# Kernel tuning notes

Measured on AMD Instinct MI355X. Metric: run time of the kernel, lower is better.

Reference implementation:

```python
import jax, jax.numpy as jnp
import numpy as np

N_NODES = 50000
N_EDGES = 500000
D = 128
R = 8
L = 2
BN_EPS = 1e-5


def setup_inputs() -> dict:
    key = jax.random.key(0)
    ks = jax.random.split(key, 8)
    x = jax.random.normal(ks[0], (N_NODES, D), dtype=jnp.float32)
    xe = jax.random.normal(ks[1], (N_EDGES, D), dtype=jnp.float32)
    edge_index = jax.random.randint(ks[2], (2, N_EDGES), 0, N_NODES, dtype=jnp.int64)
    edge_type = jax.random.randint(ks[3], (N_EDGES,), 0, R, dtype=jnp.int64)
    # glorot init for weight/root, zeros bias; BN affine params
    w_scale = jnp.sqrt(6.0 / (D + D))
    weight = jax.random.uniform(ks[4], (L, R, D, D), jnp.float32, -w_scale, w_scale)
    root = jax.random.uniform(ks[5], (L, D, D), jnp.float32, -w_scale, w_scale)
    bias = jnp.zeros((L, D), jnp.float32)
    bn_gamma = jnp.ones((L, D), jnp.float32)
    bn_beta = jnp.zeros((L, D), jnp.float32)
    return {"x": x, "xe": xe, "edge_index": edge_index, "edge_type": edge_type,
            "weight": weight, "root": root, "bias": bias,
            "bn_gamma": bn_gamma, "bn_beta": bn_beta}


def _rgcn_edge_conv(h, xe, src, dst, etype, w, rt, b):
    # message: relu(x_j + xe) per edge (independent of relation mask)
    m = jax.nn.relu(h[src] + xe)                         # [E, D]
    # mean-aggregate per (relation, dst) via a combined segment id
    n = h.shape[0]
    seg = etype * n + dst                                # [E]
    sums = jax.ops.segment_sum(m, seg, num_segments=R * n)            # [R*N, D]
    cnt = jax.ops.segment_sum(jnp.ones((m.shape[0],), m.dtype), seg,
                              num_segments=R * n)                     # [R*N]
    mean = sums / jnp.maximum(cnt, 1.0)[:, None]
    hr = mean.reshape(R, n, -1)                          # [R, N, D]
    out = jnp.einsum('rnd,rdo->no', hr, w)               # sum_i H_i @ W_i
    out = out + h @ rt + b
    return out


def _batch_norm(h, gamma, beta):
    mu = h.mean(axis=0)
    var = jnp.mean((h - mu) ** 2, axis=0)  # biased, as torch BN (training)
    return (h - mu) * jax.lax.rsqrt(var + BN_EPS) * gamma + beta


def reference(x, xe, edge_index, edge_type, weight, root, bias, bn_gamma, bn_beta):
    src, dst = edge_index[0], edge_index[1]
    h = x
    for l in range(L):
        h = _rgcn_edge_conv(h, xe, src, dst, edge_type, weight[l], root[l], bias[l])
        h = _batch_norm(h, bn_gamma[l], bn_beta[l])
        if l != L - 1:
            h = jax.nn.relu(h)
        # drop_ratio=0 -> dropout is identity
    return h  # JK='last'
```

## Files before the change

kernel.cpp:

```cpp
#include <hip/hip_runtime.h>
#include <hip/hip_bf16.h>

typedef __attribute__((ext_vector_type(8))) short bf16x8;
typedef __attribute__((ext_vector_type(4))) float f32x4;

constexpr int D = 128;
constexpr int R = 8;
constexpr float BN_EPS = 1e-5f;

__device__ __forceinline__ unsigned short f2bf(float x) {
  __hip_bfloat16 b = __float2bfloat16(x);
  union { __hip_bfloat16 b; unsigned short u; } c; c.b = b; return c.u;
}
__device__ __forceinline__ float bf2f(unsigned short u) {
  union { float f; unsigned int i; } c; c.i = ((unsigned int)u) << 16; return c.f;
}

__global__ __launch_bounds__(256) void hist_k(const int* __restrict__ ei,
                                              const int* __restrict__ et,
                                              int* __restrict__ cnt, int E) {
  int e = blockIdx.x * 256 + threadIdx.x;
  if (e >= E) return;
  atomicAdd(&cnt[ei[E + e] * 8 + et[e]], 1);
}

__global__ __launch_bounds__(256) void scan_partial_k(const int* __restrict__ cnt,
                                                      int* __restrict__ offs,
                                                      int* __restrict__ bsum, int NK) {
  __shared__ int s[256];
  int tid = threadIdx.x;
  int base = blockIdx.x * 4096 + tid * 16;
  int loc[16];
  int sum = 0;
  #pragma unroll
  for (int i = 0; i < 16; ++i) {
    int idx = base + i;
    int v = (idx < NK) ? cnt[idx] : 0;
    loc[i] = sum; sum += v;
  }
  s[tid] = sum;
  __syncthreads();
  if (tid == 0) {
    int run = 0;
    for (int i = 0; i < 256; ++i) { int t = s[i]; s[i] = run; run += t; }
    bsum[blockIdx.x] = run;
  }
  __syncthreads();
  int off = s[tid];
  #pragma unroll
  for (int i = 0; i < 16; ++i) {
    int idx = base + i;
    if (idx < NK) offs[idx] = off + loc[i];
  }
}

__global__ void scan_bsums_k(int* __restrict__ bsum, int nb) {
  if (threadIdx.x == 0 && blockIdx.x == 0) {
    int run = 0;
    for (int b = 0; b < nb; ++b) { int t = bsum[b]; bsum[b] = run; run += t; }
  }
}

__global__ __launch_bounds__(256) void scan_addback_k(int* __restrict__ offs,
                                                      const int* __restrict__ bsum,
                                                      int NK, int E) {
  int idx = blockIdx.x * 256 + threadIdx.x;
  if (idx < NK) offs[idx] += bsum[idx >> 12];
  if (idx == 0) offs[NK] = E;
}

__global__ __launch_bounds__(256) void place_k(const int* __restrict__ ei,
                                               const int* __restrict__ et,
                                               const int* __restrict__ offs,
                                               int* __restrict__ cnt,
                                               int2* __restrict__ pairs, int E) {
  int e = blockIdx.x * 256 + threadIdx.x;
  if (e >= E) return;
  int key = ei[E + e] * 8 + et[e];
  int pos = offs[key] + atomicAdd(&cnt[key], 1);
  pairs[pos] = make_int2(e, ei[e]);
}

__global__ void bnprep_k(const float* __restrict__ colstats,
                         const float* __restrict__ gamma,
                         const float* __restrict__ beta,
                         float* __restrict__ sc, float* __restrict__ sh, int N) {
  int c = threadIdx.x;
  float invN = 1.0f / (float)N;
  float mu = colstats[c] * invN;
  float var = colstats[128 + c] * invN - mu * mu;
  float scale = rsqrtf(var + BN_EPS) * gamma[c];
  sc[c] = scale;
  sh[c] = beta[c] - mu * scale;
}

__device__ __forceinline__ void edge_acc(float4& acc, int e, int s, int c, int pos,
                                         const unsigned short* __restrict__ hb,
                                         const float* __restrict__ xe) {
  float4 xv = ((const float4*)xe)[(size_t)e * 32 + c];
  ushort4 hu = *(const ushort4*)(hb + (size_t)s * 128 + pos);
  acc.x += fmaxf(xv.x + bf2f(hu.x), 0.f);
  acc.y += fmaxf(xv.y + bf2f(hu.y), 0.f);
  acc.z += fmaxf(xv.z + bf2f(hu.z), 0.f);
  acc.w += fmaxf(xv.w + bf2f(hu.w), 0.f);
}

__global__ __launch_bounds__(256) void agg_k(const unsigned short* __restrict__ hb,
                                             const float* __restrict__ xe,
                                             const int2* __restrict__ pairs,
                                             const int* __restrict__ offs,
                                             unsigned short* __restrict__ Mb,
                                             int NK, int rev) {
  int grp = threadIdx.x >> 5;
  int idx = blockIdx.x * 8 + grp;
  int nIdx = NK >> 3;
  if (idx >= nIdx) return;
  if (rev) idx = nIdx - 1 - idx;
  int s0 = idx * 8;
  int c = threadIdx.x & 31;
  int pos = (c >> 3) * 32 + (c & 3) * 8 + ((c >> 2) & 1) * 4;

  int4 ov0 = *(const int4*)(offs + s0);
  int4 ov1 = *(const int4*)(offs + s0 + 4);
  int o8 = offs[s0 + 8];
  int st[8] = {ov0.x, ov0.y, ov0.z, ov0.w, ov1.x, ov1.y, ov1.z, ov1.w};
  int en[8] = {ov0.y, ov0.z, ov0.w, ov1.x, ov1.y, ov1.z, ov1.w, o8};

  int2 pr[8];
  #pragma unroll
  for (int j = 0; j < 8; ++j) {
    int m = en[j] - st[j];
    if (m > 0) pr[j] = pairs[st[j] + min(c, min(m, 32) - 1)];
  }

  float4 acc[8];
  #pragma unroll
  for (int j = 0; j < 8; ++j) acc[j] = make_float4(0.f, 0.f, 0.f, 0.f);

#define EP(j, i) edge_acc(acc[j], __shfl(pr[j].x, (i), 32), \
                          __shfl(pr[j].y, (i), 32), c, pos, hb, xe)

  #pragma unroll
  for (int j = 0; j < 8; ++j) {
    int m = en[j] - st[j];
    if (m > 0) {
      int mm = min(m, 32);
      EP(j, 0);
      if (mm >= 2) EP(j, 1);
      if (mm >= 3) EP(j, 2);
      if (mm >= 4) EP(j, 3);
      for (int i = 4; i < mm; ++i) EP(j, i);
      for (int base = st[j] + 32; base < en[j]; base += 32) {
        int mm2 = min(32, en[j] - base);
        int2 pr2 = pairs[base + min(c, mm2 - 1)];
        for (int i = 0; i < mm2; ++i)
          edge_acc(acc[j], __shfl(pr2.x, i, 32), __shfl(pr2.y, i, 32),
                   c, pos, hb, xe);
      }
    }
  }
#undef EP

  #pragma unroll
  for (int j = 0; j < 8; ++j) {
    int len = en[j] - st[j];
    float inv = (len > 0) ? 1.0f / (float)len : 0.f;
    ushort4 u;
    u.x = f2bf(acc[j].x * inv); u.y = f2bf(acc[j].y * inv);
    u.z = f2bf(acc[j].z * inv); u.w = f2bf(acc[j].w * inv);
    *(ushort4*)(Mb + (size_t)(s0 + j) * 128 + pos) = u;
  }
}

template <int AFF>
__global__ __launch_bounds__(256) void cast_swz_k(const float* __restrict__ in,
                                                  unsigned short* __restrict__ outb,
                                                  const float* __restrict__ sc,
                                                  const float* __restrict__ sh,
                                                  int n4) {
  int gi = blockIdx.x * 256 + threadIdx.x;
  if (gi >= n4) return;
  int n = gi >> 5, c = gi & 31;
  float4 v = ((const float4*)in)[gi];
  if (AFF) {
    float4 scv = *(const float4*)(sc + c * 4);
    float4 shv = *(const float4*)(sh + c * 4);
    v.x = fmaxf(fmaf(v.x, scv.x, shv.x), 0.f);
    v.y = fmaxf(fmaf(v.y, scv.y, shv.y), 0.f);
    v.z = fmaxf(fmaf(v.z, scv.z, shv.z), 0.f);
    v.w = fmaxf(fmaf(v.w, scv.w, shv.w), 0.f);
  }
  int pos = (c >> 3) * 32 + (c & 3) * 8 + ((c >> 2) & 1) * 4;
  ushort4 u;
  u.x = f2bf(v.x); u.y = f2bf(v.y); u.z = f2bf(v.z); u.w = f2bf(v.w);
  *(ushort4*)(outb + (size_t)n * 128 + pos) = u;
}

__global__ __launch_bounds__(256) void wcast_k(const float* __restrict__ W,
                                               const float* __restrict__ root,
                                               unsigned short* __restrict__ Whi) {
  int idx = blockIdx.x * 256 + threadIdx.x;
  if (idx >= 1152 * 128) return;
  int k = idx >> 7, col = idx & 127;
  float w = (k < 1024) ? W[idx] : root[idx - 1024 * 128];
  int kk = k & 31;
  int pos = (k & ~31) + ((kk & 15) >> 2) * 8 + (kk >> 4) * 4 + (kk & 3);
  Whi[col * 1152 + pos] = f2bf(w);
}

__global__ __launch_bounds__(256) void gemm_k(
    const unsigned short* __restrict__ Mb,
    const unsigned short* __restrict__ hb,
    const unsigned short* __restrict__ Whi,
    const float* __restrict__ bias,
    float* __restrict__ out,
    float* __restrict__ colstats, int N) {
  __shared__ float ldsS[128], ldsQ[128];
  const int tid = threadIdx.x;
  const int wv = tid >> 6, lane = tid & 63;
  const int lr = lane & 15, g = lane >> 4;
  const int r0 = blockIdx.x * 128;
  const int cf0 = wv * 2;

  int row[8];
  #pragma unroll
  for (int rf = 0; rf < 8; ++rf) row[rf] = min(r0 + rf * 16 + lr, N - 1);

  const unsigned short* pb0 = Whi + (size_t)(cf0 * 16 + lr) * 1152 + g * 8;
  const unsigned short* pb1 = pb0 + 16 * 1152;

  f32x4 acc[8][2];
  #pragma unroll
  for (int a = 0; a < 8; ++a)
    #pragma unroll
    for (int b = 0; b < 2; ++b) acc[a][b] = (f32x4){0.f, 0.f, 0.f, 0.f};

  #pragma unroll 2
  for (int t = 0; t < 32; ++t) {
    bf16x8 b0 = *(const bf16x8*)(pb0 + t * 32);
    bf16x8 b1 = *(const bf16x8*)(pb1 + t * 32);
    #pragma unroll
    for (int rf = 0; rf < 8; ++rf) {
      bf16x8 a = *(const bf16x8*)(Mb + (size_t)row[rf] * 1024 + t * 32 + g * 8);
      acc[rf][0] = __builtin_amdgcn_mfma_f32_16x16x32_bf16(a, b0, acc[rf][0], 0, 0, 0);
      acc[rf][1] = __builtin_amdgcn_mfma_f32_16x16x32_bf16(a, b1, acc[rf][1], 0, 0, 0);
    }
  }
  #pragma unroll
  for (int tt = 0; tt < 4; ++tt) {
    bf16x8 b0 = *(const bf16x8*)(pb0 + 1024 + tt * 32);
    bf16x8 b1 = *(const bf16x8*)(pb1 + 1024 + tt * 32);
    #pragma unroll
    for (int rf = 0; rf < 8; ++rf) {
      bf16x8 a = *(const bf16x8*)(hb + (size_t)row[rf] * 128 + tt * 32 + g * 8);
      acc[rf][0] = __builtin_amdgcn_mfma_f32_16x16x32_bf16(a, b0, acc[rf][0], 0, 0, 0);
      acc[rf][1] = __builtin_amdgcn_mfma_f32_16x16x32_bf16(a, b1, acc[rf][1], 0, 0, 0);
    }
  }

  #pragma unroll
  for (int c = 0; c < 2; ++c) {
    int col = (cf0 + c) * 16 + lr;
    float bs = bias[col];
    float s = 0.f, q = 0.f;
    #pragma unroll
    for (int rf = 0; rf < 8; ++rf) {
      #pragma unroll
      for (int j = 0; j < 4; ++j) {
        int r = r0 + rf * 16 + g * 4 + j;
        if (r < N) {
          float v = acc[rf][c][j] + bs;
          out[(size_t)r * 128 + col] = v;
          s += v; q += v * v;
        }
      }
    }
    s += __shfl_xor(s, 16); s += __shfl_xor(s, 32);
    q += __shfl_xor(q, 16); q += __shfl_xor(q, 32);
    if (g == 0) { ldsS[col] = s; ldsQ[col] = q; }
  }
  __syncthreads();
  if (tid < 128) {
    atomicAdd(&colstats[tid], ldsS[tid]);
    atomicAdd(&colstats[128 + tid], ldsQ[tid]);
  }
}

__global__ __launch_bounds__(256) void bn_apply_k(
    const float* __restrict__ in, float* __restrict__ out,
    const float* __restrict__ colstats,
    const float* __restrict__ gamma, const float* __restrict__ beta, int N) {
  int gi = blockIdx.x * 256 + threadIdx.x;
  if (gi >= N * 32) return;
  int c0 = (gi & 31) * 4;
  float invN = 1.0f / (float)N;
  float4 v = ((const float4*)in)[gi];
  float4 o;
  #pragma unroll
  for (int j = 0; j < 4; ++j) {
    int cc = c0 + j;
    float mu = colstats[cc] * invN;
    float var = colstats[128 + cc] * invN - mu * mu;
    float scale = rsqrtf(var + BN_EPS) * gamma[cc];
    float shift = beta[cc] - mu * scale;
    float x = (j == 0) ? v.x : (j == 1) ? v.y : (j == 2) ? v.z : v.w;
    float y = x * scale + shift;
    if (j == 0) o.x = y; else if (j == 1) o.y = y; else if (j == 2) o.z = y; else o.w = y;
  }
  ((float4*)out)[gi] = o;
}

extern "C" void kernel_launch(void* const* d_in, const int* in_sizes, int n_in,
                              void* d_out, int out_size, void* d_ws, size_t ws_size,
                              hipStream_t stream) {
  const float* x      = (const float*)d_in[0];
  const float* xe     = (const float*)d_in[1];
  const int*   ei     = (const int*)d_in[2];
  const int*   et     = (const int*)d_in[3];
  const float* weight = (const float*)d_in[4];
  const float* root   = (const float*)d_in[5];
  const float* bias   = (const float*)d_in[6];
  const float* gamma  = (const float*)d_in[7];
  const float* beta   = (const float*)d_in[8];
  float* out = (float*)d_out;

  const int N = in_sizes[0] / D;
  const int E = in_sizes[3];
  const int NK = N * R;

  char* w = (char*)d_ws;
  size_t off = 0;
  auto alloc = [&](size_t bytes) { char* p = w + off; off = (off + bytes + 255) & ~(size_t)255; return p; };
  unsigned short* Mb   = (unsigned short*)alloc((size_t)NK * 128 * 2);
  unsigned short* hb   = (unsigned short*)alloc((size_t)N * 128 * 2);
  float*          h1   = (float*)alloc((size_t)N * 128 * 4);
  unsigned short* Whi  = (unsigned short*)alloc(1152 * 128 * 2);
  int*            offs = (int*)alloc((size_t)(NK + 8) * 4);
  int*            cnt  = (int*)alloc((size_t)NK * 4);
  int2*           pairs= (int2*)alloc((size_t)E * 8);
  int*            bsum = (int*)alloc(512 * 4);
  float*          cst0 = (float*)alloc(256 * 4);
  float*          cst1 = (float*)alloc(256 * 4);
  float*          sc   = (float*)alloc(128 * 4);
  float*          sh   = (float*)alloc(128 * 4);

  const int NB = (NK + 4095) / 4096;

  hipMemsetAsync(cnt, 0, (size_t)NK * 4, stream);
  hist_k<<<(E + 255) / 256, 256, 0, stream>>>(ei, et, cnt, E);
  scan_partial_k<<<NB, 256, 0, stream>>>(cnt, offs, bsum, NK);
  scan_bsums_k<<<1, 64, 0, stream>>>(bsum, NB);
  scan_addback_k<<<(NK + 255) / 256, 256, 0, stream>>>(offs, bsum, NK, E);
  hipMemsetAsync(cnt, 0, (size_t)NK * 4, stream);
  place_k<<<(E + 255) / 256, 256, 0, stream>>>(ei, et, offs, cnt, pairs, E);

  const int aggBlocks  = ((NK >> 3) + 7) / 8;
  const int gemmBlocks = (N + 127) / 128;
  const int castBlocks = (N * 32 + 255) / 256;

  wcast_k<<<576, 256, 0, stream>>>(weight, root, Whi);
  cast_swz_k<0><<<castBlocks, 256, 0, stream>>>(x, hb, nullptr, nullptr, N * 32);
  agg_k<<<aggBlocks, 256, 0, stream>>>(hb, xe, pairs, offs, Mb, NK, 0);
  hipMemsetAsync(cst0, 0, 256 * 4, stream);
  gemm_k<<<gemmBlocks, 256, 0, stream>>>(Mb, hb, Whi, bias, h1, cst0, N);
  bnprep_k<<<1, 128, 0, stream>>>(cst0, gamma, beta, sc, sh, N);

  wcast_k<<<576, 256, 0, stream>>>(weight + (size_t)1024 * 128,
                                   root + (size_t)128 * 128, Whi);
  cast_swz_k<1><<<castBlocks, 256, 0, stream>>>(h1, hb, sc, sh, N * 32);
  agg_k<<<aggBlocks, 256, 0, stream>>>(hb, xe, pairs, offs, Mb, NK, 1);
  hipMemsetAsync(cst1, 0, 256 * 4, stream);
  gemm_k<<<gemmBlocks, 256, 0, stream>>>(Mb, hb, Whi, bias + D, out, cst1, N);
  bn_apply_k<<<castBlocks, 256, 0, stream>>>(out, out, cst1, gamma + D, beta + D, N);
}
```

Baseline: 471.0 us.

## Split edge aggregation into coalesced message pass and segment reduce, gather in GEMM

Reorders segment keys to relation-major, replaces the per-segment gather kernel with a per-edge message kernel that reads xe sequentially and scatters bf16 messages into sorted slots, then a reduce kernel that only averages segments with two or more edges. The GEMM reads each relation's A rows indirectly from a zero row, the single message, or the reduced mean, avoiding writes for empty and singleton segments. This trades random xe reads for an extra bf16 message buffer write and read and indirect A loads in the GEMM.

```diff
diff --git a/kernel.cpp b/kernel.cpp
--- a/kernel.cpp
+++ b/kernel.cpp
@@ -15,13 +15,16 @@
 __device__ __forceinline__ float bf2f(unsigned short u) {
   union { float f; unsigned int i; } c; c.i = ((unsigned int)u) << 16; return c.f;
 }
+__device__ __forceinline__ int swz(int c) {
+  return (c >> 3) * 32 + (c & 3) * 8 + ((c >> 2) & 1) * 4;
+}
 
 __global__ __launch_bounds__(256) void hist_k(const int* __restrict__ ei,
                                               const int* __restrict__ et,
-                                              int* __restrict__ cnt, int E) {
+                                              int* __restrict__ cnt, int E, int N) {
   int e = blockIdx.x * 256 + threadIdx.x;
   if (e >= E) return;
-  atomicAdd(&cnt[ei[E + e] * 8 + et[e]], 1);
+  atomicAdd(&cnt[et[e] * N + ei[E + e]], 1);
 }
 
 __global__ __launch_bounds__(256) void scan_partial_k(const int* __restrict__ cnt,
@@ -73,12 +76,11 @@
                                                const int* __restrict__ et,
                                                const int* __restrict__ offs,
                                                int* __restrict__ cnt,
-                                               int2* __restrict__ pairs, int E) {
+                                               int* __restrict__ epos, int E, int N) {
   int e = blockIdx.x * 256 + threadIdx.x;
   if (e >= E) return;
-  int key = ei[E + e] * 8 + et[e];
-  int pos = offs[key] + atomicAdd(&cnt[key], 1);
-  pairs[pos] = make_int2(e, ei[e]);
+  int key = et[e] * N + ei[E + e];
+  epos[e] = offs[key] + atomicAdd(&cnt[key], 1);
 }
 
 __global__ void bnprep_k(const float* __restrict__ colstats,
@@ -94,31 +96,37 @@
   sh[c] = beta[c] - mu * scale;
 }
 
-__device__ __forceinline__ void edge_acc(float4& acc, int e, int s, int c, int pos,
-                                         const unsigned short* __restrict__ hb,
-                                         const float* __restrict__ xe) {
+__global__ __launch_bounds__(256) void msg_k(const unsigned short* __restrict__ hb,
+                                             const float* __restrict__ xe,
+                                             const int* __restrict__ ei,
+                                             const int* __restrict__ epos,
+                                             unsigned short* __restrict__ msgs, int E) {
+  int g = blockIdx.x * 256 + threadIdx.x;
+  int e = g >> 5, c = g & 31;
+  if (e >= E) return;
+  int src = ei[e];
+  int p = epos[e];
+  int pos = swz(c);
   float4 xv = ((const float4*)xe)[(size_t)e * 32 + c];
-  ushort4 hu = *(const ushort4*)(hb + (size_t)s * 128 + pos);
-  acc.x += fmaxf(xv.x + bf2f(hu.x), 0.f);
-  acc.y += fmaxf(xv.y + bf2f(hu.y), 0.f);
-  acc.z += fmaxf(xv.z + bf2f(hu.z), 0.f);
-  acc.w += fmaxf(xv.w + bf2f(hu.w), 0.f);
-}
-
-__global__ __launch_bounds__(256) void agg_k(const unsigned short* __restrict__ hb,
-                                             const float* __restrict__ xe,
-                                             const int2* __restrict__ pairs,
-                                             const int* __restrict__ offs,
-                                             unsigned short* __restrict__ Mb,
-                                             int NK, int rev) {
+  ushort4 hu = *(const ushort4*)(hb + (size_t)src * 128 + pos);
+  ushort4 u;
+  u.x = f2bf(fmaxf(xv.x + bf2f(hu.x), 0.f));
+  u.y = f2bf(fmaxf(xv.y + bf2f(hu.y), 0.f));
+  u.z = f2bf(fmaxf(xv.z + bf2f(hu.z), 0.f));
+  u.w = f2bf(fmaxf(xv.w + bf2f(hu.w), 0.f));
+  *(ushort4*)(msgs + (size_t)p * 128 + pos) = u;
+}
+
+__global__ __launch_bounds__(256) void reduce_k(const unsigned short* __restrict__ msgs,
+                                                const int* __restrict__ offs,
+                                                unsigned short* __restrict__ Mb, int NK) {
   int grp = threadIdx.x >> 5;
   int idx = blockIdx.x * 8 + grp;
   int nIdx = NK >> 3;
   if (idx >= nIdx) return;
-  if (rev) idx = nIdx - 1 - idx;
   int s0 = idx * 8;
   int c = threadIdx.x & 31;
-  int pos = (c >> 3) * 32 + (c & 3) * 8 + ((c >> 2) & 1) * 4;
+  int pos = swz(c);
 
   int4 ov0 = *(const int4*)(offs + s0);
   int4 ov1 = *(const int4*)(offs + s0 + 4);
@@ -126,49 +134,22 @@
   int st[8] = {ov0.x, ov0.y, ov0.z, ov0.w, ov1.x, ov1.y, ov1.z, ov1.w};
   int en[8] = {ov0.y, ov0.z, ov0.w, ov1.x, ov1.y, ov1.z, ov1.w, o8};
 
-  int2 pr[8];
-  #pragma unroll
-  for (int j = 0; j < 8; ++j) {
-    int m = en[j] - st[j];
-    if (m > 0) pr[j] = pairs[st[j] + min(c, min(m, 32) - 1)];
-  }
-
-  float4 acc[8];
-  #pragma unroll
-  for (int j = 0; j < 8; ++j) acc[j] = make_float4(0.f, 0.f, 0.f, 0.f);
-
-#define EP(j, i) edge_acc(acc[j], __shfl(pr[j].x, (i), 32), \
-                          __shfl(pr[j].y, (i), 32), c, pos, hb, xe)
-
-  #pragma unroll
-  for (int j = 0; j < 8; ++j) {
-    int m = en[j] - st[j];
-    if (m > 0) {
-      int mm = min(m, 32);
-      EP(j, 0);
-      if (mm >= 2) EP(j, 1);
-      if (mm >= 3) EP(j, 2);
-      if (mm >= 4) EP(j, 3);
-      for (int i = 4; i < mm; ++i) EP(j, i);
-      for (int base = st[j] + 32; base < en[j]; base += 32) {
-        int mm2 = min(32, en[j] - base);
-        int2 pr2 = pairs[base + min(c, mm2 - 1)];
-        for (int i = 0; i < mm2; ++i)
-          edge_acc(acc[j], __shfl(pr2.x, i, 32), __shfl(pr2.y, i, 32),
-                   c, pos, hb, xe);
-      }
-    }
-  }
-#undef EP
-
   #pragma unroll
   for (int j = 0; j < 8; ++j) {
     int len = en[j] - st[j];
-    float inv = (len > 0) ? 1.0f / (float)len : 0.f;
-    ushort4 u;
-    u.x = f2bf(acc[j].x * inv); u.y = f2bf(acc[j].y * inv);
-    u.z = f2bf(acc[j].z * inv); u.w = f2bf(acc[j].w * inv);
-    *(ushort4*)(Mb + (size_t)(s0 + j) * 128 + pos) = u;
+    if (len >= 2) {
+      float4 acc = make_float4(0.f, 0.f, 0.f, 0.f);
+      for (int i = st[j]; i < en[j]; ++i) {
+        ushort4 u = *(const ushort4*)(msgs + (size_t)i * 128 + pos);
+        acc.x += bf2f(u.x); acc.y += bf2f(u.y);
+        acc.z += bf2f(u.z); acc.w += bf2f(u.w);
+      }
+      float inv = 1.0f / (float)len;
+      ushort4 o;
+      o.x = f2bf(acc.x * inv); o.y = f2bf(acc.y * inv);
+      o.z = f2bf(acc.z * inv); o.w = f2bf(acc.w * inv);
+      *(ushort4*)(Mb + (size_t)(s0 + j) * 128 + pos) = o;
+    }
   }
 }
 
@@ -190,7 +171,7 @@
     v.z = fmaxf(fmaf(v.z, scv.z, shv.z), 0.f);
     v.w = fmaxf(fmaf(v.w, scv.w, shv.w), 0.f);
   }
-  int pos = (c >> 3) * 32 + (c & 3) * 8 + ((c >> 2) & 1) * 4;
+  int pos = swz(c);
   ushort4 u;
   u.x = f2bf(v.x); u.y = f2bf(v.y); u.z = f2bf(v.z); u.w = f2bf(v.w);
   *(ushort4*)(outb + (size_t)n * 128 + pos) = u;
@@ -209,7 +190,10 @@
 }
 
 __global__ __launch_bounds__(256) void gemm_k(
+    const unsigned short* __restrict__ msgs,
     const unsigned short* __restrict__ Mb,
+    const int* __restrict__ offs,
+    const unsigned short* __restrict__ zrow,
     const unsigned short* __restrict__ hb,
     const unsigned short* __restrict__ Whi,
     const float* __restrict__ bias,
@@ -235,15 +219,28 @@
     #pragma unroll
     for (int b = 0; b < 2; ++b) acc[a][b] = (f32x4){0.f, 0.f, 0.f, 0.f};
 
-  #pragma unroll 2
-  for (int t = 0; t < 32; ++t) {
-    bf16x8 b0 = *(const bf16x8*)(pb0 + t * 32);
-    bf16x8 b1 = *(const bf16x8*)(pb1 + t * 32);
+  for (int rel = 0; rel < 8; ++rel) {
+    const unsigned short* base[8];
     #pragma unroll
     for (int rf = 0; rf < 8; ++rf) {
-      bf16x8 a = *(const bf16x8*)(Mb + (size_t)row[rf] * 1024 + t * 32 + g * 8);
-      acc[rf][0] = __builtin_amdgcn_mfma_f32_16x16x32_bf16(a, b0, acc[rf][0], 0, 0, 0);
-      acc[rf][1] = __builtin_amdgcn_mfma_f32_16x16x32_bf16(a, b1, acc[rf][1], 0, 0, 0);
+      int seg = rel * N + row[rf];
+      int2 se = *(const int2*)(offs + seg);
+      int len = se.y - se.x;
+      base[rf] = (len == 0) ? zrow
+               : (len == 1) ? msgs + (size_t)se.x * 128
+                            : Mb + (size_t)seg * 128;
+    }
+    #pragma unroll
+    for (int kt = 0; kt < 4; ++kt) {
+      int t = rel * 4 + kt;
+      bf16x8 b0 = *(const bf16x8*)(pb0 + t * 32);
+      bf16x8 b1 = *(const bf16x8*)(pb1 + t * 32);
+      #pragma unroll
+      for (int rf = 0; rf < 8; ++rf) {
+        bf16x8 a = *(const bf16x8*)(base[rf] + kt * 32 + g * 8);
+        acc[rf][0] = __builtin_amdgcn_mfma_f32_16x16x32_bf16(a, b0, acc[rf][0], 0, 0, 0);
+        acc[rf][1] = __builtin_amdgcn_mfma_f32_16x16x32_bf16(a, b1, acc[rf][1], 0, 0, 0);
+      }
     }
   }
   #pragma unroll
@@ -331,45 +328,53 @@
   char* w = (char*)d_ws;
   size_t off = 0;
   auto alloc = [&](size_t bytes) { char* p = w + off; off = (off + bytes + 255) & ~(size_t)255; return p; };
+  unsigned short* msgs = (unsigned short*)alloc((size_t)E * 128 * 2);
   unsigned short* Mb   = (unsigned short*)alloc((size_t)NK * 128 * 2);
   unsigned short* hb   = (unsigned short*)alloc((size_t)N * 128 * 2);
   float*          h1   = (float*)alloc((size_t)N * 128 * 4);
   unsigned short* Whi  = (unsigned short*)alloc(1152 * 128 * 2);
   int*            offs = (int*)alloc((size_t)(NK + 8) * 4);
   int*            cnt  = (int*)alloc((size_t)NK * 4);
-  int2*           pairs= (int2*)alloc((size_t)E * 8);
+  int*            epos = (int*)alloc((size_t)E * 4);
   int*            bsum = (int*)alloc(512 * 4);
   float*          cst0 = (float*)alloc(256 * 4);
   float*          cst1 = (float*)alloc(256 * 4);
   float*          sc   = (float*)alloc(128 * 4);
   float*          sh   = (float*)alloc(128 * 4);
+  unsigned short* zrow = (unsigned short*)alloc(256);
 
   const int NB = (NK + 4095) / 4096;
 
   hipMemsetAsync(cnt, 0, (size_t)NK * 4, stream);
-  hist_k<<<(E + 255) / 256, 256, 0, stream>>>(ei, et, cnt, E);
+  hipMemsetAsync(zrow, 0, 256, stream);
+  hist_k<<<(E + 255) / 256, 256, 0, stream>>>(ei, et, cnt, E, N);
   scan_partial_k<<<NB, 256, 0, stream>>>(cnt, offs, bsum, NK);
   scan_bsums_k<<<1, 64, 0, stream>>>(bsum, NB);
   scan_addback_k<<<(NK + 255) / 256, 256, 0, stream>>>(offs, bsum, NK, E);
   hipMemsetAsync(cnt, 0, (size_t)NK * 4, stream);
-  place_k<<<(E + 255) / 256, 256, 0, stream>>>(ei, et, offs, cnt, pairs, E);
-
-  const int aggBlocks  = ((NK >> 3) + 7) / 8;
+  place_k<<<(E + 255) / 256, 256, 0, stream>>>(ei, et, offs, cnt, epos, E, N);
+
+  const int msgBlocks  = (E * 32 + 255) / 256;
+  const int redBlocks  = ((NK >> 3) + 7) / 8;
   const int gemmBlocks = (N + 127) / 128;
   const int castBlocks = (N * 32 + 255) / 256;
 
   wcast_k<<<576, 256, 0, stream>>>(weight, root, Whi);
   cast_swz_k<0><<<castBlocks, 256, 0, stream>>>(x, hb, nullptr, nullptr, N * 32);
-  agg_k<<<aggBlocks, 256, 0, stream>>>(hb, xe, pairs, offs, Mb, NK, 0);
+  msg_k<<<msgBlocks, 256, 0, stream>>>(hb, xe, ei, epos, msgs, E);
+  reduce_k<<<redBlocks, 256, 0, stream>>>(msgs, offs, Mb, NK);
   hipMemsetAsync(cst0, 0, 256 * 4, stream);
-  gemm_k<<<gemmBlocks, 256, 0, stream>>>(Mb, hb, Whi, bias, h1, cst0, N);
+  gemm_k<<<gemmBlocks, 256, 0, stream>>>(msgs, Mb, offs, zrow, hb, Whi,
+                                         bias, h1, cst0, N);
   bnprep_k<<<1, 128, 0, stream>>>(cst0, gamma, beta, sc, sh, N);
 
   wcast_k<<<576, 256, 0, stream>>>(weight + (size_t)1024 * 128,
                                    root + (size_t)128 * 128, Whi);
   cast_swz_k<1><<<castBlocks, 256, 0, stream>>>(h1, hb, sc, sh, N * 32);
-  agg_k<<<aggBlocks, 256, 0, stream>>>(hb, xe, pairs, offs, Mb, NK, 1);
+  msg_k<<<msgBlocks, 256, 0, stream>>>(hb, xe, ei, epos, msgs, E);
+  reduce_k<<<redBlocks, 256, 0, stream>>>(msgs, offs, Mb, NK);
   hipMemsetAsync(cst1, 0, 256 * 4, stream);
-  gemm_k<<<gemmBlocks, 256, 0, stream>>>(Mb, hb, Whi, bias + D, out, cst1, N);
+  gemm_k<<<gemmBlocks, 256, 0, stream>>>(msgs, Mb, offs, zrow, hb, Whi,
+                                         bias + D, out, cst1, N);
   bn_apply_k<<<castBlocks, 256, 0, stream>>>(out, out, cst1, gamma + D, beta + D, N);
 }
```

After: 598.8 us. +27.1%, slower.

## Pre-permute edge features into sorted bf16 order for contiguous aggregation reads

Applied to the files above, without the earlier changes.

Adds a kernel that writes xe once in CSR-sorted edge order as swizzled bf16. Both aggregation passes can then read edge features contiguously at half the bytes instead of gathering fp32 rows by edge id. The pairs array becomes a plain source-index array, and the reversed traversal in the second layer is dropped. The cost is an extra full pass over xe (read 256MB, scattered write 128MB), a large workspace buffer, and bf16 rounding of xe.

```diff
diff --git a/kernel.cpp b/kernel.cpp
--- a/kernel.cpp
+++ b/kernel.cpp
@@ -14,6 +14,9 @@
 }
 __device__ __forceinline__ float bf2f(unsigned short u) {
   union { float f; unsigned int i; } c; c.i = ((unsigned int)u) << 16; return c.f;
+}
+__device__ __forceinline__ int swz(int c) {
+  return (c >> 3) * 32 + (c & 3) * 8 + ((c >> 2) & 1) * 4;
 }
 
 __global__ __launch_bounds__(256) void hist_k(const int* __restrict__ ei,
@@ -73,12 +76,28 @@
                                                const int* __restrict__ et,
                                                const int* __restrict__ offs,
                                                int* __restrict__ cnt,
-                                               int2* __restrict__ pairs, int E) {
+                                               int* __restrict__ srcs,
+                                               int* __restrict__ epos, int E) {
   int e = blockIdx.x * 256 + threadIdx.x;
   if (e >= E) return;
   int key = ei[E + e] * 8 + et[e];
   int pos = offs[key] + atomicAdd(&cnt[key], 1);
-  pairs[pos] = make_int2(e, ei[e]);
+  srcs[pos] = ei[e];
+  epos[e] = pos;
+}
+
+__global__ __launch_bounds__(256) void xeperm_k(const float* __restrict__ xe,
+                                                const int* __restrict__ epos,
+                                                unsigned short* __restrict__ xes, int E) {
+  int g = blockIdx.x * 256 + threadIdx.x;
+  int e = g >> 5, c = g & 31;
+  if (e >= E) return;
+  int p = epos[e];
+  float4 xv = ((const float4*)xe)[(size_t)e * 32 + c];
+  int pos = swz(c);
+  ushort4 u;
+  u.x = f2bf(xv.x); u.y = f2bf(xv.y); u.z = f2bf(xv.z); u.w = f2bf(xv.w);
+  *(ushort4*)(xes + (size_t)p * 128 + pos) = u;
 }
 
 __global__ void bnprep_k(const float* __restrict__ colstats,
@@ -94,31 +113,29 @@
   sh[c] = beta[c] - mu * scale;
 }
 
-__device__ __forceinline__ void edge_acc(float4& acc, int e, int s, int c, int pos,
+__device__ __forceinline__ void edge_acc(float4& acc, int i, int s, int pos,
                                          const unsigned short* __restrict__ hb,
-                                         const float* __restrict__ xe) {
-  float4 xv = ((const float4*)xe)[(size_t)e * 32 + c];
+                                         const unsigned short* __restrict__ xes) {
+  ushort4 xu = *(const ushort4*)(xes + (size_t)i * 128 + pos);
   ushort4 hu = *(const ushort4*)(hb + (size_t)s * 128 + pos);
-  acc.x += fmaxf(xv.x + bf2f(hu.x), 0.f);
-  acc.y += fmaxf(xv.y + bf2f(hu.y), 0.f);
-  acc.z += fmaxf(xv.z + bf2f(hu.z), 0.f);
-  acc.w += fmaxf(xv.w + bf2f(hu.w), 0.f);
+  acc.x += fmaxf(bf2f(xu.x) + bf2f(hu.x), 0.f);
+  acc.y += fmaxf(bf2f(xu.y) + bf2f(hu.y), 0.f);
+  acc.z += fmaxf(bf2f(xu.z) + bf2f(hu.z), 0.f);
+  acc.w += fmaxf(bf2f(xu.w) + bf2f(hu.w), 0.f);
 }
 
 __global__ __launch_bounds__(256) void agg_k(const unsigned short* __restrict__ hb,
-                                             const float* __restrict__ xe,
-                                             const int2* __restrict__ pairs,
+                                             const unsigned short* __restrict__ xes,
+                                             const int* __restrict__ srcs,
                                              const int* __restrict__ offs,
-                                             unsigned short* __restrict__ Mb,
-                                             int NK, int rev) {
+                                             unsigned short* __restrict__ Mb, int NK) {
   int grp = threadIdx.x >> 5;
   int idx = blockIdx.x * 8 + grp;
   int nIdx = NK >> 3;
   if (idx >= nIdx) return;
-  if (rev) idx = nIdx - 1 - idx;
   int s0 = idx * 8;
   int c = threadIdx.x & 31;
-  int pos = (c >> 3) * 32 + (c & 3) * 8 + ((c >> 2) & 1) * 4;
+  int pos = swz(c);
 
   int4 ov0 = *(const int4*)(offs + s0);
   int4 ov1 = *(const int4*)(offs + s0 + 4);
@@ -126,19 +143,18 @@
   int st[8] = {ov0.x, ov0.y, ov0.z, ov0.w, ov1.x, ov1.y, ov1.z, ov1.w};
   int en[8] = {ov0.y, ov0.z, ov0.w, ov1.x, ov1.y, ov1.z, ov1.w, o8};
 
-  int2 pr[8];
+  int sv[8];
   #pragma unroll
   for (int j = 0; j < 8; ++j) {
     int m = en[j] - st[j];
-    if (m > 0) pr[j] = pairs[st[j] + min(c, min(m, 32) - 1)];
+    if (m > 0) sv[j] = srcs[st[j] + min(c, min(m, 32) - 1)];
   }
 
   float4 acc[8];
   #pragma unroll
   for (int j = 0; j < 8; ++j) acc[j] = make_float4(0.f, 0.f, 0.f, 0.f);
 
-#define EP(j, i) edge_acc(acc[j], __shfl(pr[j].x, (i), 32), \
-                          __shfl(pr[j].y, (i), 32), c, pos, hb, xe)
+#define EP(j, i) edge_acc(acc[j], st[j] + (i), __shfl(sv[j], (i), 32), pos, hb, xes)
 
   #pragma unroll
   for (int j = 0; j < 8; ++j) {
@@ -152,10 +168,9 @@
       for (int i = 4; i < mm; ++i) EP(j, i);
       for (int base = st[j] + 32; base < en[j]; base += 32) {
         int mm2 = min(32, en[j] - base);
-        int2 pr2 = pairs[base + min(c, mm2 - 1)];
+        int sv2 = srcs[base + min(c, mm2 - 1)];
         for (int i = 0; i < mm2; ++i)
-          edge_acc(acc[j], __shfl(pr2.x, i, 32), __shfl(pr2.y, i, 32),
-                   c, pos, hb, xe);
+          edge_acc(acc[j], base + i, __shfl(sv2, i, 32), pos, hb, xes);
       }
     }
   }
@@ -190,7 +205,7 @@
     v.z = fmaxf(fmaf(v.z, scv.z, shv.z), 0.f);
     v.w = fmaxf(fmaf(v.w, scv.w, shv.w), 0.f);
   }
-  int pos = (c >> 3) * 32 + (c & 3) * 8 + ((c >> 2) & 1) * 4;
+  int pos = swz(c);
   ushort4 u;
   u.x = f2bf(v.x); u.y = f2bf(v.y); u.z = f2bf(v.z); u.w = f2bf(v.w);
   *(ushort4*)(outb + (size_t)n * 128 + pos) = u;
@@ -331,13 +346,15 @@
   char* w = (char*)d_ws;
   size_t off = 0;
   auto alloc = [&](size_t bytes) { char* p = w + off; off = (off + bytes + 255) & ~(size_t)255; return p; };
+  unsigned short* xes  = (unsigned short*)alloc((size_t)E * 128 * 2);
   unsigned short* Mb   = (unsigned short*)alloc((size_t)NK * 128 * 2);
   unsigned short* hb   = (unsigned short*)alloc((size_t)N * 128 * 2);
   float*          h1   = (float*)alloc((size_t)N * 128 * 4);
   unsigned short* Whi  = (unsigned short*)alloc(1152 * 128 * 2);
   int*            offs = (int*)alloc((size_t)(NK + 8) * 4);
   int*            cnt  = (int*)alloc((size_t)NK * 4);
-  int2*           pairs= (int2*)alloc((size_t)E * 8);
+  int*            srcs = (int*)alloc((size_t)E * 4);
+  int*            epos = (int*)alloc((size_t)E * 4);
   int*            bsum = (int*)alloc(512 * 4);
   float*          cst0 = (float*)alloc(256 * 4);
   float*          cst1 = (float*)alloc(256 * 4);
@@ -352,7 +369,8 @@
   scan_bsums_k<<<1, 64, 0, stream>>>(bsum, NB);
   scan_addback_k<<<(NK + 255) / 256, 256, 0, stream>>>(offs, bsum, NK, E);
   hipMemsetAsync(cnt, 0, (size_t)NK * 4, stream);
-  place_k<<<(E + 255) / 256, 256, 0, stream>>>(ei, et, offs, cnt, pairs, E);
+  place_k<<<(E + 255) / 256, 256, 0, stream>>>(ei, et, offs, cnt, srcs, epos, E);
+  xeperm_k<<<(E * 32 + 255) / 256, 256, 0, stream>>>(xe, epos, xes, E);
 
   const int aggBlocks  = ((NK >> 3) + 7) / 8;
   const int gemmBlocks = (N + 127) / 128;
@@ -360,7 +378,7 @@
 
   wcast_k<<<576, 256, 0, stream>>>(weight, root, Whi);
   cast_swz_k<0><<<castBlocks, 256, 0, stream>>>(x, hb, nullptr, nullptr, N * 32);
-  agg_k<<<aggBlocks, 256, 0, stream>>>(hb, xe, pairs, offs, Mb, NK, 0);
+  agg_k<<<aggBlocks, 256, 0, stream>>>(hb, xes, srcs, offs, Mb, NK);
   hipMemsetAsync(cst0, 0, 256 * 4, stream);
   gemm_k<<<gemmBlocks, 256, 0, stream>>>(Mb, hb, Whi, bias, h1, cst0, N);
   bnprep_k<<<1, 128, 0, stream>>>(cst0, gamma, beta, sc, sh, N);
@@ -368,7 +386,7 @@
   wcast_k<<<576, 256, 0, stream>>>(weight + (size_t)1024 * 128,
                                    root + (size_t)128 * 128, Whi);
   cast_swz_k<1><<<castBlocks, 256, 0, stream>>>(h1, hb, sc, sh, N * 32);
-  agg_k<<<aggBlocks, 256, 0, stream>>>(hb, xe, pairs, offs, Mb, NK, 1);
+  agg_k<<<aggBlocks, 256, 0, stream>>>(hb, xes, srcs, offs, Mb, NK);
   hipMemsetAsync(cst1, 0, 256 * 4, stream);
   gemm_k<<<gemmBlocks, 256, 0, stream>>>(Mb, hb, Whi, bias + D, out, cst1, N);
   bn_apply_k<<<castBlocks, 256, 0, stream>>>(out, out, cst1, gamma + D, beta + D, N);
```

After: 511.8 us. +8.7%, slower.
